# Performance work log

Hardware: AMD Instinct MI355X
Metric: run time of the kernel (lower is better)

## Reference

```python
import jax, jax.numpy as jnp
import numpy as np

B, N, F, H, OUT = 64, 512, 128, 256, 6


def setup_inputs() -> dict:
    key = jax.random.key(0)
    ks = jax.random.split(key, 20)
    s = 0.02
    inp = {
        "x": jax.random.normal(ks[0], (B * N, F), dtype=jnp.float32),
        "edge_index": jax.random.randint(ks[1], (2, 16), 0, B * N),
        "edge_weight": jax.random.uniform(ks[2], (16,), dtype=jnp.float32),
        "batch": jnp.repeat(jnp.arange(B, dtype=jnp.int64), N),
        "sigma": jax.random.uniform(ks[3], (1,), dtype=jnp.float32),
        "Wg": s * jax.random.normal(ks[4], (F, F)), "bg": jnp.zeros((F,)),
        "Wrel0": s * jax.random.normal(ks[5], (F, H)), "Wroot0": s * jax.random.normal(ks[6], (F, H)), "brel0": jnp.zeros((H,)),
        "Wrel1": s * jax.random.normal(ks[7], (H, H)), "Wroot1": s * jax.random.normal(ks[8], (H, H)), "brel1": jnp.zeros((H,)),
        "Wrel2": s * jax.random.normal(ks[9], (H, H)), "Wroot2": s * jax.random.normal(ks[10], (H, H)), "brel2": jnp.zeros((H,)),
        "W1": s * jax.random.normal(ks[11], (H, H)), "b1": jnp.zeros((H,)),
        "Wout": s * jax.random.normal(ks[12], (H, OUT)), "bout": jnp.zeros((OUT,)),
    }
    return inp


def _forward(x, sigma, Wg, bg, Wrel0, Wroot0, brel0, Wrel1, Wroot1, brel1,
             Wrel2, Wroot2, brel2, W1, b1, Wout, bout):
    # gdmLinear
    h = x @ Wg + bg                      # [B*N, F]
    hw = h.reshape(B, N, -1)             # to_dense_batch (equal-size windows)
    # pairwise squared distances per window -> Gaussian kernel
    sq = jnp.sum(hw * hw, axis=-1)       # [B, N]
    dist = jnp.maximum(sq[:, :, None] + sq[:, None, :]
                       - 2.0 * jnp.einsum('bnf,bmf->bnm', hw, hw), 0.0)
    A = jnp.exp(-dist / (2.0 * sigma[0] ** 2))   # [B, N, N], all > 0
    A = A * (1.0 - jnp.eye(N, dtype=A.dtype))    # nonzero extraction drops self-loops

    def conv(h, Wrel, Wroot, brel):
        # GraphConv: out_i = W_rel @ sum_j A[j,i] * h_j + b_rel + W_root @ h_i
        agg = jnp.einsum('bji,bjf->bif', A, h)
        return agg @ Wrel + brel + h @ Wroot

    h = hw
    h = jax.nn.relu(conv(h, Wrel0, Wroot0, brel0))
    h = jax.nn.relu(conv(h, Wrel1, Wroot1, brel1))
    h = conv(h, Wrel2, Wroot2, brel2)
    g = jnp.mean(h, axis=1)              # global_mean_pool (equal-size graphs)
    g = jax.nn.relu(g @ W1 + b1)
    return g @ Wout + bout               # [B, OUT]


def reference(x, edge_index, edge_weight, batch, sigma, Wg, bg,
              Wrel0, Wroot0, brel0, Wrel1, Wroot1, brel1,
              Wrel2, Wroot2, brel2, W1, b1, Wout, bout):
    # edge_index / edge_weight / batch inputs are recomputed internally by GdmGNN
    return _forward(x, sigma, Wg, bg, Wrel0, Wroot0, brel0, Wrel1, Wroot1, brel1,
                    Wrel2, Wroot2, brel2, W1, b1, Wout, bout)
```

## Files before the change

### kernel.cpp

```cpp
#include <hip/hip_runtime.h>
#include <math.h>

#define Bsz 64
#define Nn 512
#define Ff 128
#define Hh 256
#define OUTD 6
#define MTOT (Bsz * Nn)

typedef __bf16 bf16x8 __attribute__((ext_vector_type(8)));
typedef float f32x4 __attribute__((ext_vector_type(4)));
typedef int int4v __attribute__((ext_vector_type(4)));
typedef unsigned short ushort4v __attribute__((ext_vector_type(4)));

__device__ __forceinline__ unsigned short f2bf(float f) {
    unsigned u = __float_as_uint(f);
    u += 0x7FFFu + ((u >> 16) & 1u);
    return (unsigned short)(u >> 16);
}
__device__ __forceinline__ float bf2f(unsigned short s) {
    return __uint_as_float(((unsigned)s) << 16);
}

#define SWZ(r) (((r) ^ ((r) >> 2)) & 3)

__device__ __forceinline__ void async_ld16(const unsigned short* g, unsigned short* l) {
    __builtin_amdgcn_global_load_lds(
        (const __attribute__((address_space(1))) void*)g,
        (__attribute__((address_space(3))) void*)l,
        16, 0, 0);
}

#define LDH 40
#define TSZ (128 * 32)
#define AGP 136

__global__ __launch_bounds__(512) void gemm_ah(
    const unsigned short* __restrict__ HT, const unsigned short* __restrict__ Arows,
    unsigned short* __restrict__ agg,
    int F, long strideHT, long strideA, long strideC, int mTiles)
{
    int id = blockIdx.x;
    int bz = id & 63;
    int t = id >> 6;
    int bx = t % mTiles;
    int by = t / mTiles;

    HT += (long)bz * strideHT;
    Arows += (long)bz * strideA;
    agg += (long)bz * strideC;

    __shared__ unsigned short As[2 * TSZ];
    __shared__ unsigned short Bs[2 * TSZ];

    int tid = threadIdx.x;
    int lane = tid & 63;
    int wave = tid >> 6;
    int quad = lane >> 4, l16 = lane & 15;
    int wm = (wave >> 1) * 32, wn = (wave & 1) * 64;
    int m0 = bx * 128, n0 = by * 128;

    int sr = lane >> 2, sc = lane & 3;

    f32x4 acc[2][4] = {};

    auto issue = [&](int g) {
        int kk = g << 5;
        unsigned short* Ad = As + (g & 1) * TSZ;
        unsigned short* Bd = Bs + (g & 1) * TSZ;
        int r = wave * 16 + sr;
        int c = sc ^ SWZ(r);
        async_ld16(HT + (long)(m0 + r) * Nn + kk + c * 8, Ad + (wave * 16) * 32);
        async_ld16(Arows + (long)(n0 + r) * Nn + kk + c * 8, Bd + (wave * 16) * 32);
    };

    issue(0);
    for (int g = 0; g < (Nn >> 5); ++g) {
        __syncthreads();
        if (g + 1 < (Nn >> 5)) issue(g + 1);
        const unsigned short* Ab = As + (g & 1) * TSZ;
        const unsigned short* Bb = Bs + (g & 1) * TSZ;
        bf16x8 af[2], bfr[4];
        #pragma unroll
        for (int i = 0; i < 2; ++i) {
            int r = wm + i * 16 + l16;
            af[i] = *(const bf16x8*)&Ab[r * 32 + (quad ^ SWZ(r)) * 8];
        }
        #pragma unroll
        for (int j = 0; j < 4; ++j) {
            int r = wn + j * 16 + l16;
            bfr[j] = *(const bf16x8*)&Bb[r * 32 + (quad ^ SWZ(r)) * 8];
        }
        #pragma unroll
        for (int i = 0; i < 2; ++i)
            #pragma unroll
            for (int j = 0; j < 4; ++j)
                acc[i][j] = __builtin_amdgcn_mfma_f32_16x16x32_bf16(
                    af[i], bfr[j], acc[i][j], 0, 0, 0);
    }

    #pragma unroll
    for (int i = 0; i < 2; ++i) {
        int f = m0 + wm + i * 16 + quad * 4;
        #pragma unroll
        for (int j = 0; j < 4; ++j) {
            int node = n0 + wn + j * 16 + l16;
            f32x4 v = acc[i][j];
            ushort4v p;
            p[0] = f2bf(v[0]); p[1] = f2bf(v[1]); p[2] = f2bf(v[2]); p[3] = f2bf(v[3]);
            *(ushort4v*)&agg[(long)node * F + f] = p;
        }
    }
}

__global__ __launch_bounds__(512) void fused_l0(
    const unsigned short* __restrict__ h0T,
    const unsigned short* __restrict__ Arows,
    const unsigned short* __restrict__ h0b,
    const unsigned short* __restrict__ WrelT0,
    const unsigned short* __restrict__ WrootT0,
    const float* __restrict__ brel0,
    unsigned short* __restrict__ h1b,
    unsigned short* __restrict__ h1T)
{
    int id = blockIdx.x;
    int b = id & 63;
    int nt = id >> 6;
    int n0g = nt * 128;
    long nodeBase = (long)b * Nn + n0g;

    const unsigned short* HT = h0T + (long)b * Ff * Nn;
    const unsigned short* AR = Arows + (long)b * Nn * Nn;

    __shared__ unsigned short SA[2 * TSZ];
    __shared__ unsigned short SB[2 * TSZ];
    __shared__ unsigned short aggL[128 * AGP];

    int tid = threadIdx.x;
    int lane = tid & 63;
    int wave = tid >> 6;
    int quad = lane >> 4, l16 = lane & 15;
    int wm = (wave >> 1) * 32, wn = (wave & 1) * 64;
    int sr = lane >> 2, sc = lane & 3;

    {
        f32x4 acc[2][4] = {};
        auto issue = [&](int g) {
            int kk = g << 5;
            unsigned short* Ad = SA + (g & 1) * TSZ;
            unsigned short* Bd = SB + (g & 1) * TSZ;
            int r = wave * 16 + sr;
            int c = sc ^ SWZ(r);
            async_ld16(HT + (long)r * Nn + kk + c * 8, Ad + (wave * 16) * 32);
            async_ld16(AR + (long)(n0g + r) * Nn + kk + c * 8, Bd + (wave * 16) * 32);
        };
        issue(0);
        for (int g = 0; g < (Nn >> 5); ++g) {
            __syncthreads();
            if (g + 1 < (Nn >> 5)) issue(g + 1);
            const unsigned short* Ab = SA + (g & 1) * TSZ;
            const unsigned short* Bb = SB + (g & 1) * TSZ;
            bf16x8 af[2], bfr[4];
            #pragma unroll
            for (int i = 0; i < 2; ++i) {
                int r = wm + i * 16 + l16;
                af[i] = *(const bf16x8*)&Ab[r * 32 + (quad ^ SWZ(r)) * 8];
            }
            #pragma unroll
            for (int j = 0; j < 4; ++j) {
                int r = wn + j * 16 + l16;
                bfr[j] = *(const bf16x8*)&Bb[r * 32 + (quad ^ SWZ(r)) * 8];
            }
            #pragma unroll
            for (int i = 0; i < 2; ++i)
                #pragma unroll
                for (int j = 0; j < 4; ++j)
                    acc[i][j] = __builtin_amdgcn_mfma_f32_16x16x32_bf16(
                        af[i], bfr[j], acc[i][j], 0, 0, 0);
        }
        #pragma unroll
        for (int i = 0; i < 2; ++i) {
            int f = wm + i * 16 + quad * 4;
            #pragma unroll
            for (int j = 0; j < 4; ++j) {
                int nl = wn + j * 16 + l16;
                f32x4 v = acc[i][j];
                ushort4v p;
                p[0] = f2bf(v[0]); p[1] = f2bf(v[1]);
                p[2] = f2bf(v[2]); p[3] = f2bf(v[3]);
                *(ushort4v*)&aggL[nl * AGP + f] = p;
            }
        }
    }
    __syncthreads();

    for (int half = 0; half < 2; ++half) {
        int m0 = half * 128;
        f32x4 acc[2][4] = {};
        auto issue = [&](int g) {
            unsigned short* Ad = SA + (g & 1) * TSZ;
            int r = wave * 16 + sr;
            int c = sc ^ SWZ(r);
            if (g < 4) {
                async_ld16(WrelT0 + (long)(m0 + r) * Ff + (g << 5) + c * 8,
                           Ad + (wave * 16) * 32);
            } else {
                async_ld16(WrootT0 + (long)(m0 + r) * Ff + ((g - 4) << 5) + c * 8,
                           Ad + (wave * 16) * 32);
                unsigned short* Bd = SB + (g & 1) * TSZ;
                async_ld16(h0b + (nodeBase + r) * Ff + ((g - 4) << 5) + c * 8,
                           Bd + (wave * 16) * 32);
            }
        };
        issue(0);
        for (int g = 0; g < 8; ++g) {
            __syncthreads();
            if (g + 1 < 8) issue(g + 1);
            const unsigned short* Ab = SA + (g & 1) * TSZ;
            bf16x8 af[2], bfr[4];
            #pragma unroll
            for (int i = 0; i < 2; ++i) {
                int r = wm + i * 16 + l16;
                af[i] = *(const bf16x8*)&Ab[r * 32 + (quad ^ SWZ(r)) * 8];
            }
            if (g < 4) {
                #pragma unroll
                for (int j = 0; j < 4; ++j) {
                    int nl = wn + j * 16 + l16;
                    bfr[j] = *(const bf16x8*)&aggL[nl * AGP + (g << 5) + quad * 8];
                }
            } else {
                const unsigned short* Bb = SB + (g & 1) * TSZ;
                #pragma unroll
                for (int j = 0; j < 4; ++j) {
                    int r = wn + j * 16 + l16;
                    bfr[j] = *(const bf16x8*)&Bb[r * 32 + (quad ^ SWZ(r)) * 8];
                }
            }
            #pragma unroll
            for (int i = 0; i < 2; ++i)
                #pragma unroll
                for (int j = 0; j < 4; ++j)
                    acc[i][j] = __builtin_amdgcn_mfma_f32_16x16x32_bf16(
                        af[i], bfr[j], acc[i][j], 0, 0, 0);
        }
        #pragma unroll
        for (int i = 0; i < 2; ++i) {
            int of = m0 + wm + i * 16 + quad * 4;
            float b0 = brel0[of + 0], b1 = brel0[of + 1];
            float b2 = brel0[of + 2], b3 = brel0[of + 3];
            #pragma unroll
            for (int j = 0; j < 4; ++j) {
                int nl = wn + j * 16 + l16;
                f32x4 v = acc[i][j];
                float o0 = fmaxf(v[0] + b0, 0.f), o1 = fmaxf(v[1] + b1, 0.f);
                float o2 = fmaxf(v[2] + b2, 0.f), o3 = fmaxf(v[3] + b3, 0.f);
                ushort4v p;
                p[0] = f2bf(o0); p[1] = f2bf(o1); p[2] = f2bf(o2); p[3] = f2bf(o3);
                *(ushort4v*)&h1b[(nodeBase + nl) * Hh + of] = p;
                long base = ((long)b * Hh) * 512 + n0g + nl;
                h1T[base + (long)(of + 0) * 512] = p[0];
                h1T[base + (long)(of + 1) * 512] = p[1];
                h1T[base + (long)(of + 2) * 512] = p[2];
                h1T[base + (long)(of + 3) * 512] = p[3];
            }
        }
    }
}

__global__ __launch_bounds__(512) void dense_pool(
    const unsigned short* __restrict__ A0, const unsigned short* __restrict__ B0T,
    const unsigned short* __restrict__ A1, const unsigned short* __restrict__ B1T,
    const float* __restrict__ bias,
    const float* __restrict__ w, float* __restrict__ vpart, float* __restrict__ mpart,
    int K0, int K1)
{
    int m0 = blockIdx.x * 128;
    int n0 = blockIdx.y * 128;

    __shared__ unsigned short As[2 * TSZ];
    __shared__ unsigned short Bs[2 * TSZ];
    __shared__ float vred[128];
    __shared__ float mred[128];

    int tid = threadIdx.x;
    int lane = tid & 63;
    int wave = tid >> 6;
    int quad = lane >> 4, l16 = lane & 15;
    int wm = (wave >> 1) * 32, wn = (wave & 1) * 64;

    int sr = lane >> 2, sc = lane & 3;

    int T0 = K0 >> 5, T1 = K1 >> 5;
    int T = T0 + T1;

    f32x4 acc[2][4] = {};

    auto issue = [&](int g) {
        const unsigned short* Ag; const unsigned short* Bg; int Kg, kk;
        if (g < T0) { Ag = A0; Bg = B0T; Kg = K0; kk = g << 5; }
        else        { Ag = A1; Bg = B1T; Kg = K1; kk = (g - T0) << 5; }
        unsigned short* Ad = As + (g & 1) * TSZ;
        unsigned short* Bd = Bs + (g & 1) * TSZ;
        int r = wave * 16 + sr;
        int c = sc ^ SWZ(r);
        async_ld16(Ag + (long)(m0 + r) * Kg + kk + c * 8, Ad + (wave * 16) * 32);
        async_ld16(Bg + (long)(n0 + r) * Kg + kk + c * 8, Bd + (wave * 16) * 32);
    };

    issue(0);
    for (int g = 0; g < T; ++g) {
        __syncthreads();
        if (g + 1 < T) issue(g + 1);
        const unsigned short* Ab = As + (g & 1) * TSZ;
        const unsigned short* Bb = Bs + (g & 1) * TSZ;
        bf16x8 af[2], bfr[4];
        #pragma unroll
        for (int i = 0; i < 2; ++i) {
            int r = wm + i * 16 + l16;
            af[i] = *(const bf16x8*)&Ab[r * 32 + (quad ^ SWZ(r)) * 8];
        }
        #pragma unroll
        for (int j = 0; j < 4; ++j) {
            int r = wn + j * 16 + l16;
            bfr[j] = *(const bf16x8*)&Bb[r * 32 + (quad ^ SWZ(r)) * 8];
        }
        #pragma unroll
        for (int i = 0; i < 2; ++i)
            #pragma unroll
            for (int j = 0; j < 4; ++j)
                acc[i][j] = __builtin_amdgcn_mfma_f32_16x16x32_bf16(
                    af[i], bfr[j], acc[i][j], 0, 0, 0);
    }

    if (tid < 128) { vred[tid] = 0.f; mred[tid] = 0.f; }
    __syncthreads();

    #pragma unroll
    for (int i = 0; i < 2; ++i) {
        int lf = wm + i * 16 + quad * 4;
        int of = m0 + lf;
        float b0 = bias[of + 0], b1 = bias[of + 1];
        float b2 = bias[of + 2], b3 = bias[of + 3];
        float vp0 = 0.f, vp1 = 0.f, vp2 = 0.f, vp3 = 0.f;
        float mp0 = 0.f, mp1 = 0.f, mp2 = 0.f, mp3 = 0.f;
        #pragma unroll
        for (int j = 0; j < 4; ++j) {
            int node = n0 + wn + j * 16 + l16;
            f32x4 v = acc[i][j];
            float o0 = fmaxf(v[0] + b0, 0.f), o1 = fmaxf(v[1] + b1, 0.f);
            float o2 = fmaxf(v[2] + b2, 0.f), o3 = fmaxf(v[3] + b3, 0.f);
            float h0v = bf2f(f2bf(o0)), h1v = bf2f(f2bf(o1));
            float h2v = bf2f(f2bf(o2)), h3v = bf2f(f2bf(o3));
            float wv = w[node];
            vp0 += wv * h0v; vp1 += wv * h1v; vp2 += wv * h2v; vp3 += wv * h3v;
            mp0 += h0v; mp1 += h1v; mp2 += h2v; mp3 += h3v;
        }
        #pragma unroll
        for (int m = 1; m < 16; m <<= 1) {
            vp0 += __shfl_xor(vp0, m); vp1 += __shfl_xor(vp1, m);
            vp2 += __shfl_xor(vp2, m); vp3 += __shfl_xor(vp3, m);
            mp0 += __shfl_xor(mp0, m); mp1 += __shfl_xor(mp1, m);
            mp2 += __shfl_xor(mp2, m); mp3 += __shfl_xor(mp3, m);
        }
        if (l16 == 0) {
            atomicAdd(&vred[lf + 0], vp0); atomicAdd(&vred[lf + 1], vp1);
            atomicAdd(&vred[lf + 2], vp2); atomicAdd(&vred[lf + 3], vp3);
            atomicAdd(&mred[lf + 0], mp0); atomicAdd(&mred[lf + 1], mp1);
            atomicAdd(&mred[lf + 2], mp2); atomicAdd(&mred[lf + 3], mp3);
        }
    }
    __syncthreads();
    if (tid < 128) {
        long o = (long)blockIdx.y * Hh + m0 + tid;
        vpart[o] = vred[tid];
        mpart[o] = mred[tid];
    }
}

__global__ __launch_bounds__(256) void prep_h0(
    const float* __restrict__ x, const float* __restrict__ Wg,
    const float* __restrict__ bg,
    const float* __restrict__ Wrel0, const float* __restrict__ Wroot0,
    const float* __restrict__ Wrel1, const float* __restrict__ Wroot1,
    unsigned short* __restrict__ T0, unsigned short* __restrict__ T1,
    unsigned short* __restrict__ T2, unsigned short* __restrict__ T3,
    float* __restrict__ w,
    unsigned short* __restrict__ h0b, unsigned short* __restrict__ h0T,
    float* __restrict__ sqv)
{
    if (blockIdx.x < 896) {
        int idx = blockIdx.x * 256 + threadIdx.x;
        if (idx >= 196608) { w[idx - 196608] = 0.f; return; }
        const float* src; unsigned short* dst; int kin; int e;
        if      (idx <  32768) { src = Wrel0;  dst = T0; kin = 128; e = idx; }
        else if (idx <  65536) { src = Wroot0; dst = T1; kin = 128; e = idx - 32768; }
        else if (idx < 131072) { src = Wrel1;  dst = T2; kin = 256; e = idx - 65536; }
        else                   { src = Wroot1; dst = T3; kin = 256; e = idx - 131072; }
        int o = (kin == 128) ? (e >> 7) : (e >> 8);
        int i = e & (kin - 1);
        dst[e] = f2bf(src[(long)i * 256 + o]);
        return;
    }

    __shared__ unsigned short As[128 * LDH];
    __shared__ unsigned short Bs[128 * LDH];
    __shared__ float rsq[128];

    int tid = threadIdx.x;
    int lane = tid & 63;
    int wave = tid >> 6;
    int quad = lane >> 4, l16 = lane & 15;
    int wm = (wave >> 1) * 64, wn = (wave & 1) * 64;
    int m0 = (blockIdx.x - 896) * 128;

    f32x4 acc[4][4] = {};

    for (int k0 = 0; k0 < Ff; k0 += 32) {
        __syncthreads();
        #pragma unroll
        for (int l = 0; l < 2; ++l) {
            int idx = tid + l * 256;
            int r = idx >> 2, ch = idx & 3;
            const float* px = x + (long)(m0 + r) * Ff + k0 + ch * 8;
            float4 xa = *(const float4*)px;
            float4 xb = *(const float4*)(px + 4);
            ushort4v pa, pb;
            pa[0] = f2bf(xa.x); pa[1] = f2bf(xa.y); pa[2] = f2bf(xa.z); pa[3] = f2bf(xa.w);
            pb[0] = f2bf(xb.x); pb[1] = f2bf(xb.y); pb[2] = f2bf(xb.z); pb[3] = f2bf(xb.w);
            *(ushort4v*)&As[r * LDH + ch * 8] = pa;
            *(ushort4v*)&As[r * LDH + ch * 8 + 4] = pb;
            int kk = k0 + ch * 8;
            ushort4v qa, qb;
            #pragma unroll
            for (int u = 0; u < 4; ++u) qa[u] = f2bf(Wg[(long)(kk + u) * 128 + r]);
            #pragma unroll
            for (int u = 0; u < 4; ++u) qb[u] = f2bf(Wg[(long)(kk + 4 + u) * 128 + r]);
            *(ushort4v*)&Bs[r * LDH + ch * 8] = qa;
            *(ushort4v*)&Bs[r * LDH + ch * 8 + 4] = qb;
        }
        __syncthreads();
        bf16x8 af[4], bfr[4];
        #pragma unroll
        for (int i = 0; i < 4; ++i)
            af[i] = *(const bf16x8*)&As[(wm + i * 16 + l16) * LDH + quad * 8];
        #pragma unroll
        for (int j = 0; j < 4; ++j)
            bfr[j] = *(const bf16x8*)&Bs[(wn + j * 16 + l16) * LDH + quad * 8];
        #pragma unroll
        for (int i = 0; i < 4; ++i)
            #pragma unroll
            for (int j = 0; j < 4; ++j)
                acc[i][j] = __builtin_amdgcn_mfma_f32_16x16x32_bf16(
                    af[i], bfr[j], acc[i][j], 0, 0, 0);
    }

    if (tid < 128) rsq[tid] = 0.f;
    __syncthreads();

    #pragma unroll
    for (int i = 0; i < 4; ++i) {
        int lrow = wm + i * 16 + quad * 4;
        int mb = m0 + lrow;
        float rp0 = 0.f, rp1 = 0.f, rp2 = 0.f, rp3 = 0.f;
        #pragma unroll
        for (int j = 0; j < 4; ++j) {
            int n = wn + j * 16 + l16;
            f32x4 v = acc[i][j];
            float bv = bg[n];
            unsigned short s0 = f2bf(v[0] + bv), s1 = f2bf(v[1] + bv);
            unsigned short s2 = f2bf(v[2] + bv), s3 = f2bf(v[3] + bv);
            h0b[(long)(mb + 0) * Ff + n] = s0;
            h0b[(long)(mb + 1) * Ff + n] = s1;
            h0b[(long)(mb + 2) * Ff + n] = s2;
            h0b[(long)(mb + 3) * Ff + n] = s3;
            ushort4v p; p[0] = s0; p[1] = s1; p[2] = s2; p[3] = s3;
            long ti = ((long)(mb >> 9) * Ff + n) * 512 + (mb & 511);
            *(ushort4v*)&h0T[ti] = p;
            float f0 = bf2f(s0), f1 = bf2f(s1), f2 = bf2f(s2), f3 = bf2f(s3);
            rp0 += f0 * f0; rp1 += f1 * f1; rp2 += f2 * f2; rp3 += f3 * f3;
        }
        #pragma unroll
        for (int m = 1; m < 16; m <<= 1) {
            rp0 += __shfl_xor(rp0, m);
            rp1 += __shfl_xor(rp1, m);
            rp2 += __shfl_xor(rp2, m);
            rp3 += __shfl_xor(rp3, m);
        }
        if (l16 == 0) {
            atomicAdd(&rsq[lrow + 0], rp0);
            atomicAdd(&rsq[lrow + 1], rp1);
            atomicAdd(&rsq[lrow + 2], rp2);
            atomicAdd(&rsq[lrow + 3], rp3);
        }
    }
    __syncthreads();
    if (tid < 128) sqv[m0 + tid] = rsq[tid];
}

__global__ __launch_bounds__(512) void gram_A_mfma(
    const unsigned short* __restrict__ h0b, const float* __restrict__ sqv,
    const float* __restrict__ sigma, unsigned short* __restrict__ Aout,
    float* __restrict__ w)
{
    int id = blockIdx.x;
    int b = id & 63;
    int t = id >> 6;
    int i0 = (t & 3) * 128, j0 = (t >> 2) * 128;

    const unsigned short* H = h0b + (long)b * Nn * Ff;
    const float* SQ = sqv + (long)b * Nn;
    unsigned short* Ab = Aout + (long)b * Nn * Nn;

    __shared__ unsigned short Is[2 * TSZ];
    __shared__ unsigned short Js[2 * TSZ];
    __shared__ float rsum[128];

    int tid = threadIdx.x;
    int lane = tid & 63;
    int wave = tid >> 6;
    int quad = lane >> 4, l16 = lane & 15;
    int wm = (wave >> 1) * 32, wn = (wave & 1) * 64;

    int sr = lane >> 2, sc = lane & 3;

    f32x4 acc[2][4] = {};

    auto issue = [&](int g) {
        int kk = g << 5;
        unsigned short* Id = Is + (g & 1) * TSZ;
        unsigned short* Jd = Js + (g & 1) * TSZ;
        int r = wave * 16 + sr;
        int c = sc ^ SWZ(r);
        async_ld16(H + (long)(i0 + r) * Ff + kk + c * 8, Id + (wave * 16) * 32);
        async_ld16(H + (long)(j0 + r) * Ff + kk + c * 8, Jd + (wave * 16) * 32);
    };

    issue(0);
    for (int g = 0; g < (Ff >> 5); ++g) {
        __syncthreads();
        if (g + 1 < (Ff >> 5)) issue(g + 1);
        const unsigned short* Ib = Is + (g & 1) * TSZ;
        const unsigned short* Jb = Js + (g & 1) * TSZ;
        bf16x8 af[2], bfr[4];
        #pragma unroll
        for (int i = 0; i < 2; ++i) {
            int r = wm + i * 16 + l16;
            af[i] = *(const bf16x8*)&Ib[r * 32 + (quad ^ SWZ(r)) * 8];
        }
        #pragma unroll
        for (int j = 0; j < 4; ++j) {
            int r = wn + j * 16 + l16;
            bfr[j] = *(const bf16x8*)&Jb[r * 32 + (quad ^ SWZ(r)) * 8];
        }
        #pragma unroll
        for (int i = 0; i < 2; ++i)
            #pragma unroll
            for (int j = 0; j < 4; ++j)
                acc[i][j] = __builtin_amdgcn_mfma_f32_16x16x32_bf16(
                    af[i], bfr[j], acc[i][j], 0, 0, 0);
    }

    if (tid < 128) rsum[tid] = 0.f;
    __syncthreads();

    float s = sigma[0];
    float inv2s2 = 1.0f / (2.0f * s * s);
    #pragma unroll
    for (int i = 0; i < 2; ++i) {
        int lrow = wm + i * 16 + quad * 4;
        int rb = i0 + lrow;
        float rs0 = 0.f, rs1 = 0.f, rs2 = 0.f, rs3 = 0.f;
        #pragma unroll
        for (int j = 0; j < 4; ++j) {
            int c = j0 + wn + j * 16 + l16;
            float sqc = SQ[c];
            f32x4 v = acc[i][j];
            ushort4v pk;
            float av[4];
            #pragma unroll
            for (int r4 = 0; r4 < 4; ++r4) {
                int r = rb + r4;
                float d = fmaxf(SQ[r] + sqc - 2.0f * v[r4], 0.0f);
                unsigned short a = (r == c) ? (unsigned short)0
                                            : f2bf(__expf(-d * inv2s2));
                pk[r4] = a;
                av[r4] = bf2f(a);
            }
            *(ushort4v*)&Ab[(long)c * Nn + rb] = pk;
            rs0 += av[0]; rs1 += av[1]; rs2 += av[2]; rs3 += av[3];
        }
        #pragma unroll
        for (int m = 1; m < 16; m <<= 1) {
            rs0 += __shfl_xor(rs0, m);
            rs1 += __shfl_xor(rs1, m);
            rs2 += __shfl_xor(rs2, m);
            rs3 += __shfl_xor(rs3, m);
        }
        if (l16 == 0) {
            atomicAdd(&rsum[lrow + 0], rs0);
            atomicAdd(&rsum[lrow + 1], rs1);
            atomicAdd(&rsum[lrow + 2], rs2);
            atomicAdd(&rsum[lrow + 3], rs3);
        }
    }
    __syncthreads();
    if (tid < 128) atomicAdd(&w[(long)b * Nn + i0 + tid], rsum[tid]);
}

__global__ __launch_bounds__(256) void head_kernel(
    const float* __restrict__ vpart, const float* __restrict__ mpart,
    const float* __restrict__ Wrel2, const float* __restrict__ Wroot2,
    const float* __restrict__ brel2,
    const float* __restrict__ W1, const float* __restrict__ b1,
    const float* __restrict__ Wout, const float* __restrict__ bout,
    float* __restrict__ out)
{
    int b = blockIdx.x;
    int j = threadIdx.x;
    __shared__ float vs[Hh], ms[Hh], gs[Hh], g2[Hh];
    float vp = 0.f, mp = 0.f;
    #pragma unroll
    for (int p = 0; p < 4; ++p) {
        long o = ((long)(b * 4 + p)) * Hh + j;
        vp += vpart[o];
        mp += mpart[o];
    }
    vs[j] = vp * (1.0f / (float)Nn);
    ms[j] = mp * (1.0f / (float)Nn);
    __syncthreads();
    float s = brel2[j];
    for (int c = 0; c < Hh; ++c)
        s += vs[c] * Wrel2[c * Hh + j] + ms[c] * Wroot2[c * Hh + j];
    gs[j] = s;
    __syncthreads();
    float t = b1[j];
    for (int k = 0; k < Hh; ++k) t += gs[k] * W1[k * Hh + j];
    g2[j] = fmaxf(t, 0.f);
    __syncthreads();
    if (j < OUTD) {
        float s2 = bout[j];
        for (int k = 0; k < Hh; ++k) s2 += g2[k] * Wout[k * OUTD + j];
        out[b * OUTD + j] = s2;
    }
}

extern "C" void kernel_launch(void* const* d_in, const int* in_sizes, int n_in,
                              void* d_out, int out_size, void* d_ws, size_t ws_size,
                              hipStream_t stream) {
    const float* x      = (const float*)d_in[0];
    const float* sigma  = (const float*)d_in[4];
    const float* Wg     = (const float*)d_in[5];
    const float* bg     = (const float*)d_in[6];
    const float* Wrel0  = (const float*)d_in[7];
    const float* Wroot0 = (const float*)d_in[8];
    const float* brel0  = (const float*)d_in[9];
    const float* Wrel1  = (const float*)d_in[10];
    const float* Wroot1 = (const float*)d_in[11];
    const float* brel1  = (const float*)d_in[12];
    const float* Wrel2  = (const float*)d_in[13];
    const float* Wroot2 = (const float*)d_in[14];
    const float* brel2  = (const float*)d_in[15];
    const float* W1     = (const float*)d_in[16];
    const float* b1     = (const float*)d_in[17];
    const float* Wout   = (const float*)d_in[18];
    const float* bout   = (const float*)d_in[19];
    float* out = (float*)d_out;

    char* ws = (char*)d_ws;
    unsigned short* h0b  = (unsigned short*)(ws + 16777216);
    unsigned short* h0T  = (unsigned short*)(ws + 25165824);
    float*          sq   = (float*)(ws + 33554432);
    unsigned short* Aadj = (unsigned short*)(ws + 33685504);
    unsigned short* agg  = (unsigned short*)(ws + 67239936);
    unsigned short* h1b  = (unsigned short*)(ws + 84017152);
    unsigned short* h1T  = (unsigned short*)(ws + 100794368);
    unsigned short* WrelT0  = (unsigned short*)(ws + 167903232);
    unsigned short* WrootT0 = (unsigned short*)(ws + 167968768);
    unsigned short* WrelT1  = (unsigned short*)(ws + 168034304);
    unsigned short* WrootT1 = (unsigned short*)(ws + 168165376);
    float*          w     = (float*)(ws + 168558592);
    float*          vpart = (float*)(ws + 168689664);
    float*          mpart = (float*)(ws + 168951808);

    prep_h0<<<1152, 256, 0, stream>>>(x, Wg, bg, Wrel0, Wroot0, Wrel1, Wroot1,
                                      WrelT0, WrootT0, WrelT1, WrootT1,
                                      w, h0b, h0T, sq);

    gram_A_mfma<<<dim3(16 * Bsz, 1, 1), 512, 0, stream>>>(h0b, sq, sigma, Aadj, w);

    fused_l0<<<dim3(4 * Bsz, 1, 1), 512, 0, stream>>>(
        h0T, Aadj, h0b, WrelT0, WrootT0, brel0, h1b, h1T);

    gemm_ah<<<dim3(8 * Bsz, 1, 1), 512, 0, stream>>>(
        h1T, Aadj, agg, Hh,
        (long)Hh * Nn, (long)Nn * Nn, (long)Nn * Hh, 2);
    dense_pool<<<dim3(2, MTOT / 128), 512, 0, stream>>>(
        WrelT1, agg, WrootT1, h1b, brel1,
        w, vpart, mpart, Hh, Hh);

    head_kernel<<<Bsz, 256, 0, stream>>>(vpart, mpart, Wrel2, Wroot2, brel2,
                                         W1, b1, Wout, bout, out);
}
```

Measured before the change: 224.0 us.

## Fuse layer-1 aggregation GEMM with dense projection and pooling in one kernel

Replaces the separate A^T·h aggregation kernel and the dense_pool kernel for layer 1 with a single fused_l1 kernel. Each block computes a 64-node by 256-feature aggregation tile, keeps it in LDS, then multiplies it by the transposed weights and reduces the pooling partials directly. This removes the global round trip of the agg buffer and one kernel launch. In exchange it uses more LDS per block, reloads weight tiles for every 64-node tile, writes 8 pooling partials per graph instead of 4, and leaves only 512 blocks.

```diff
diff --git a/kernel.cpp b/kernel.cpp
--- a/kernel.cpp
+++ b/kernel.cpp
@@ -34,84 +34,7 @@
 #define LDH 40
 #define TSZ (128 * 32)
 #define AGP 136
-
-__global__ __launch_bounds__(512) void gemm_ah(
-    const unsigned short* __restrict__ HT, const unsigned short* __restrict__ Arows,
-    unsigned short* __restrict__ agg,
-    int F, long strideHT, long strideA, long strideC, int mTiles)
-{
-    int id = blockIdx.x;
-    int bz = id & 63;
-    int t = id >> 6;
-    int bx = t % mTiles;
-    int by = t / mTiles;
-
-    HT += (long)bz * strideHT;
-    Arows += (long)bz * strideA;
-    agg += (long)bz * strideC;
-
-    __shared__ unsigned short As[2 * TSZ];
-    __shared__ unsigned short Bs[2 * TSZ];
-
-    int tid = threadIdx.x;
-    int lane = tid & 63;
-    int wave = tid >> 6;
-    int quad = lane >> 4, l16 = lane & 15;
-    int wm = (wave >> 1) * 32, wn = (wave & 1) * 64;
-    int m0 = bx * 128, n0 = by * 128;
-
-    int sr = lane >> 2, sc = lane & 3;
-
-    f32x4 acc[2][4] = {};
-
-    auto issue = [&](int g) {
-        int kk = g << 5;
-        unsigned short* Ad = As + (g & 1) * TSZ;
-        unsigned short* Bd = Bs + (g & 1) * TSZ;
-        int r = wave * 16 + sr;
-        int c = sc ^ SWZ(r);
-        async_ld16(HT + (long)(m0 + r) * Nn + kk + c * 8, Ad + (wave * 16) * 32);
-        async_ld16(Arows + (long)(n0 + r) * Nn + kk + c * 8, Bd + (wave * 16) * 32);
-    };
-
-    issue(0);
-    for (int g = 0; g < (Nn >> 5); ++g) {
-        __syncthreads();
-        if (g + 1 < (Nn >> 5)) issue(g + 1);
-        const unsigned short* Ab = As + (g & 1) * TSZ;
-        const unsigned short* Bb = Bs + (g & 1) * TSZ;
-        bf16x8 af[2], bfr[4];
-        #pragma unroll
-        for (int i = 0; i < 2; ++i) {
-            int r = wm + i * 16 + l16;
-            af[i] = *(const bf16x8*)&Ab[r * 32 + (quad ^ SWZ(r)) * 8];
-        }
-        #pragma unroll
-        for (int j = 0; j < 4; ++j) {
-            int r = wn + j * 16 + l16;
-            bfr[j] = *(const bf16x8*)&Bb[r * 32 + (quad ^ SWZ(r)) * 8];
-        }
-        #pragma unroll
-        for (int i = 0; i < 2; ++i)
-            #pragma unroll
-            for (int j = 0; j < 4; ++j)
-                acc[i][j] = __builtin_amdgcn_mfma_f32_16x16x32_bf16(
-                    af[i], bfr[j], acc[i][j], 0, 0, 0);
-    }
-
-    #pragma unroll
-    for (int i = 0; i < 2; ++i) {
-        int f = m0 + wm + i * 16 + quad * 4;
-        #pragma unroll
-        for (int j = 0; j < 4; ++j) {
-            int node = n0 + wn + j * 16 + l16;
-            f32x4 v = acc[i][j];
-            ushort4v p;
-            p[0] = f2bf(v[0]); p[1] = f2bf(v[1]); p[2] = f2bf(v[2]); p[3] = f2bf(v[3]);
-            *(ushort4v*)&agg[(long)node * F + f] = p;
-        }
-    }
-}
+#define AGP1 264
 
 __global__ __launch_bounds__(512) void fused_l0(
     const unsigned short* __restrict__ h0T,
@@ -268,62 +191,136 @@
     }
 }
 
-__global__ __launch_bounds__(512) void dense_pool(
-    const unsigned short* __restrict__ A0, const unsigned short* __restrict__ B0T,
-    const unsigned short* __restrict__ A1, const unsigned short* __restrict__ B1T,
-    const float* __restrict__ bias,
-    const float* __restrict__ w, float* __restrict__ vpart, float* __restrict__ mpart,
-    int K0, int K1)
+__global__ __launch_bounds__(512) void fused_l1(
+    const unsigned short* __restrict__ h1T,
+    const unsigned short* __restrict__ Arows,
+    const unsigned short* __restrict__ h1b,
+    const unsigned short* __restrict__ WrelT1,
+    const unsigned short* __restrict__ WrootT1,
+    const float* __restrict__ brel1,
+    const float* __restrict__ w,
+    float* __restrict__ vpart, float* __restrict__ mpart)
 {
-    int m0 = blockIdx.x * 128;
-    int n0 = blockIdx.y * 128;
-
-    __shared__ unsigned short As[2 * TSZ];
-    __shared__ unsigned short Bs[2 * TSZ];
-    __shared__ float vred[128];
-    __shared__ float mred[128];
+    constexpr int ATS = 256 * 32;
+    constexpr int BTS = 64 * 32;
+
+    int id = blockIdx.x;
+    int b = id & 63;
+    int nt = id >> 6;
+    int n0g = nt * 64;
+    long nodeBase = (long)b * Nn + n0g;
+
+    const unsigned short* HT = h1T + (long)b * Hh * Nn;
+    const unsigned short* AR = Arows + (long)b * Nn * Nn;
+
+    __shared__ unsigned short SA[2 * ATS];
+    __shared__ unsigned short SB[2 * BTS];
+    __shared__ unsigned short aggL[64 * AGP1];
 
     int tid = threadIdx.x;
     int lane = tid & 63;
     int wave = tid >> 6;
     int quad = lane >> 4, l16 = lane & 15;
-    int wm = (wave >> 1) * 32, wn = (wave & 1) * 64;
-
+    int wm = wave * 32;
     int sr = lane >> 2, sc = lane & 3;
 
-    int T0 = K0 >> 5, T1 = K1 >> 5;
-    int T = T0 + T1;
+    {
+        f32x4 acc[2][4] = {};
+        auto issue = [&](int g) {
+            int kk = g << 5;
+            unsigned short* Ad = SA + (g & 1) * ATS;
+            int r = wave * 16 + sr;
+            int c = sc ^ SWZ(r);
+            async_ld16(HT + (long)r * Nn + kk + c * 8, Ad + (wave * 16) * 32);
+            int r2 = 128 + r;
+            int c2 = sc ^ SWZ(r2);
+            async_ld16(HT + (long)r2 * Nn + kk + c2 * 8, Ad + (128 + wave * 16) * 32);
+            if (wave < 4) {
+                unsigned short* Bd = SB + (g & 1) * BTS;
+                async_ld16(AR + (long)(n0g + r) * Nn + kk + c * 8,
+                           Bd + (wave * 16) * 32);
+            }
+        };
+        issue(0);
+        for (int g = 0; g < 16; ++g) {
+            __syncthreads();
+            if (g + 1 < 16) issue(g + 1);
+            const unsigned short* Ab = SA + (g & 1) * ATS;
+            const unsigned short* Bb = SB + (g & 1) * BTS;
+            bf16x8 af[2], bfr[4];
+            #pragma unroll
+            for (int i = 0; i < 2; ++i) {
+                int r = wm + i * 16 + l16;
+                af[i] = *(const bf16x8*)&Ab[r * 32 + (quad ^ SWZ(r)) * 8];
+            }
+            #pragma unroll
+            for (int j = 0; j < 4; ++j) {
+                int r = j * 16 + l16;
+                bfr[j] = *(const bf16x8*)&Bb[r * 32 + (quad ^ SWZ(r)) * 8];
+            }
+            #pragma unroll
+            for (int i = 0; i < 2; ++i)
+                #pragma unroll
+                for (int j = 0; j < 4; ++j)
+                    acc[i][j] = __builtin_amdgcn_mfma_f32_16x16x32_bf16(
+                        af[i], bfr[j], acc[i][j], 0, 0, 0);
+        }
+        #pragma unroll
+        for (int i = 0; i < 2; ++i) {
+            int f = wm + i * 16 + quad * 4;
+            #pragma unroll
+            for (int j = 0; j < 4; ++j) {
+                int nl = j * 16 + l16;
+                f32x4 v = acc[i][j];
+                ushort4v p;
+                p[0] = f2bf(v[0]); p[1] = f2bf(v[1]);
+                p[2] = f2bf(v[2]); p[3] = f2bf(v[3]);
+                *(ushort4v*)&aggL[nl * AGP1 + f] = p;
+            }
+        }
+    }
+    __syncthreads();
 
     f32x4 acc[2][4] = {};
-
-    auto issue = [&](int g) {
-        const unsigned short* Ag; const unsigned short* Bg; int Kg, kk;
-        if (g < T0) { Ag = A0; Bg = B0T; Kg = K0; kk = g << 5; }
-        else        { Ag = A1; Bg = B1T; Kg = K1; kk = (g - T0) << 5; }
-        unsigned short* Ad = As + (g & 1) * TSZ;
-        unsigned short* Bd = Bs + (g & 1) * TSZ;
+    auto issue2 = [&](int g) {
+        const unsigned short* Wp = (g < 8) ? WrelT1 : WrootT1;
+        int kk = (g & 7) << 5;
+        unsigned short* Ad = SA + (g & 1) * ATS;
         int r = wave * 16 + sr;
         int c = sc ^ SWZ(r);
-        async_ld16(Ag + (long)(m0 + r) * Kg + kk + c * 8, Ad + (wave * 16) * 32);
-        async_ld16(Bg + (long)(n0 + r) * Kg + kk + c * 8, Bd + (wave * 16) * 32);
+        async_ld16(Wp + (long)r * Hh + kk + c * 8, Ad + (wave * 16) * 32);
+        int r2 = 128 + r;
+        int c2 = sc ^ SWZ(r2);
+        async_ld16(Wp + (long)r2 * Hh + kk + c2 * 8, Ad + (128 + wave * 16) * 32);
+        if (g >= 8 && wave < 4) {
+            unsigned short* Bd = SB + (g & 1) * BTS;
+            async_ld16(h1b + (nodeBase + r) * Hh + kk + c * 8, Bd + (wave * 16) * 32);
+        }
     };
-
-    issue(0);
-    for (int g = 0; g < T; ++g) {
+    issue2(0);
+    for (int g = 0; g < 16; ++g) {
         __syncthreads();
-        if (g + 1 < T) issue(g + 1);
-        const unsigned short* Ab = As + (g & 1) * TSZ;
-        const unsigned short* Bb = Bs + (g & 1) * TSZ;
+        if (g + 1 < 16) issue2(g + 1);
+        const unsigned short* Ab = SA + (g & 1) * ATS;
         bf16x8 af[2], bfr[4];
         #pragma unroll
         for (int i = 0; i < 2; ++i) {
             int r = wm + i * 16 + l16;
             af[i] = *(const bf16x8*)&Ab[r * 32 + (quad ^ SWZ(r)) * 8];
         }
-        #pragma unroll
-        for (int j = 0; j < 4; ++j) {
-            int r = wn + j * 16 + l16;
-            bfr[j] = *(const bf16x8*)&Bb[r * 32 + (quad ^ SWZ(r)) * 8];
+        if (g < 8) {
+            #pragma unroll
+            for (int j = 0; j < 4; ++j) {
+                int nl = j * 16 + l16;
+                bfr[j] = *(const bf16x8*)&aggL[nl * AGP1 + (g << 5) + quad * 8];
+            }
+        } else {
+            const unsigned short* Bb = SB + (g & 1) * BTS;
+            #pragma unroll
+            for (int j = 0; j < 4; ++j) {
+                int r = j * 16 + l16;
+                bfr[j] = *(const bf16x8*)&Bb[r * 32 + (quad ^ SWZ(r)) * 8];
+            }
         }
         #pragma unroll
         for (int i = 0; i < 2; ++i)
@@ -333,20 +330,16 @@
                     af[i], bfr[j], acc[i][j], 0, 0, 0);
     }
 
-    if (tid < 128) { vred[tid] = 0.f; mred[tid] = 0.f; }
-    __syncthreads();
-
     #pragma unroll
     for (int i = 0; i < 2; ++i) {
         int lf = wm + i * 16 + quad * 4;
-        int of = m0 + lf;
-        float b0 = bias[of + 0], b1 = bias[of + 1];
-        float b2 = bias[of + 2], b3 = bias[of + 3];
+        float b0 = brel1[lf + 0], b1 = brel1[lf + 1];
+        float b2 = brel1[lf + 2], b3 = brel1[lf + 3];
         float vp0 = 0.f, vp1 = 0.f, vp2 = 0.f, vp3 = 0.f;
         float mp0 = 0.f, mp1 = 0.f, mp2 = 0.f, mp3 = 0.f;
         #pragma unroll
         for (int j = 0; j < 4; ++j) {
-            int node = n0 + wn + j * 16 + l16;
+            long node = nodeBase + j * 16 + l16;
             f32x4 v = acc[i][j];
             float o0 = fmaxf(v[0] + b0, 0.f), o1 = fmaxf(v[1] + b1, 0.f);
             float o2 = fmaxf(v[2] + b2, 0.f), o3 = fmaxf(v[3] + b3, 0.f);
@@ -364,17 +357,12 @@
             mp2 += __shfl_xor(mp2, m); mp3 += __shfl_xor(mp3, m);
         }
         if (l16 == 0) {
-            atomicAdd(&vred[lf + 0], vp0); atomicAdd(&vred[lf + 1], vp1);
-            atomicAdd(&vred[lf + 2], vp2); atomicAdd(&vred[lf + 3], vp3);
-            atomicAdd(&mred[lf + 0], mp0); atomicAdd(&mred[lf + 1], mp1);
-            atomicAdd(&mred[lf + 2], mp2); atomicAdd(&mred[lf + 3], mp3);
-        }
-    }
-    __syncthreads();
-    if (tid < 128) {
-        long o = (long)blockIdx.y * Hh + m0 + tid;
-        vpart[o] = vred[tid];
-        mpart[o] = mred[tid];
+            long o = ((long)(b * 8 + nt)) * Hh + lf;
+            float4 vv = {vp0, vp1, vp2, vp3};
+            float4 mm = {mp0, mp1, mp2, mp3};
+            *(float4*)&vpart[o] = vv;
+            *(float4*)&mpart[o] = mm;
+        }
     }
 }
 
@@ -621,8 +609,8 @@
     __shared__ float vs[Hh], ms[Hh], gs[Hh], g2[Hh];
     float vp = 0.f, mp = 0.f;
     #pragma unroll
-    for (int p = 0; p < 4; ++p) {
-        long o = ((long)(b * 4 + p)) * Hh + j;
+    for (int p = 0; p < 8; ++p) {
+        long o = ((long)(b * 8 + p)) * Hh + j;
         vp += vpart[o];
         mp += mpart[o];
     }
@@ -672,7 +660,6 @@
     unsigned short* h0T  = (unsigned short*)(ws + 25165824);
     float*          sq   = (float*)(ws + 33554432);
     unsigned short* Aadj = (unsigned short*)(ws + 33685504);
-    unsigned short* agg  = (unsigned short*)(ws + 67239936);
     unsigned short* h1b  = (unsigned short*)(ws + 84017152);
     unsigned short* h1T  = (unsigned short*)(ws + 100794368);
     unsigned short* WrelT0  = (unsigned short*)(ws + 167903232);
@@ -681,7 +668,7 @@
     unsigned short* WrootT1 = (unsigned short*)(ws + 168165376);
     float*          w     = (float*)(ws + 168558592);
     float*          vpart = (float*)(ws + 168689664);
-    float*          mpart = (float*)(ws + 168951808);
+    float*          mpart = (float*)(ws + 169213952);
 
     prep_h0<<<1152, 256, 0, stream>>>(x, Wg, bg, Wrel0, Wroot0, Wrel1, Wroot1,
                                       WrelT0, WrootT0, WrelT1, WrootT1,
@@ -692,12 +679,8 @@
     fused_l0<<<dim3(4 * Bsz, 1, 1), 512, 0, stream>>>(
         h0T, Aadj, h0b, WrelT0, WrootT0, brel0, h1b, h1T);
 
-    gemm_ah<<<dim3(8 * Bsz, 1, 1), 512, 0, stream>>>(
-        h1T, Aadj, agg, Hh,
-        (long)Hh * Nn, (long)Nn * Nn, (long)Nn * Hh, 2);
-    dense_pool<<<dim3(2, MTOT / 128), 512, 0, stream>>>(
-        WrelT1, agg, WrootT1, h1b, brel1,
-        w, vpart, mpart, Hh, Hh);
+    fused_l1<<<dim3(8 * Bsz, 1, 1), 512, 0, stream>>>(
+        h1T, Aadj, h1b, WrelT1, WrootT1, brel1, w, vpart, mpart);
 
     head_kernel<<<Bsz, 256, 0, stream>>>(vpart, mpart, Wrel2, Wroot2, brel2,
                                          W1, b1, Wout, bout, out);
```

After: 213.4 us, median of 2. 1.05x faster.
